# Kernel tuning notes

Measured on AMD Instinct MI355X. Metric: run time of the kernel, lower is better.

## Reference

```python
import jax, jax.numpy as jnp
import numpy as np

B, T, C = 4, 2048, 1024
H, D = 16, 64           # num_heads, head_size
R = D // 2              # rotary_ndims = 32


def _make_rope(T, R):
    # RotaryEmbedding(dim=R): inv_freq over arange(0, R, 2)
    inv_freq = 1.0 / (10000.0 ** (np.arange(0, R, 2, dtype=np.float32) / R))
    t = np.arange(T, dtype=np.float32)
    freqs = np.einsum('i,j->ij', t, inv_freq)        # [T, R/2]
    emb = np.concatenate([freqs, freqs], axis=-1)    # [T, R]
    return jnp.asarray(np.stack([np.cos(emb), np.sin(emb)]), dtype=jnp.float32)  # [2, T, R]


def setup_inputs() -> dict:
    key = jax.random.key(0)
    ks = jax.random.split(key, 10)
    s = 1.0 / np.sqrt(C)
    inp = {
        'x': jax.random.normal(ks[0], (B, T, C), dtype=jnp.float32),
        'RoPE': _make_rope(T, R),
        'key_padding_mask': jax.random.randint(ks[1], (B, T), 0, 2, dtype=jnp.int32),
        'Wq': jax.random.normal(ks[2], (C, C), dtype=jnp.float32) * s,
        'bq': jnp.zeros((C,), dtype=jnp.float32),
        'Wk': jax.random.normal(ks[3], (C, C), dtype=jnp.float32) * s,
        'bk': jnp.zeros((C,), dtype=jnp.float32),
        'Wv': jax.random.normal(ks[4], (C, C), dtype=jnp.float32) * s,
        'bv': jnp.zeros((C,), dtype=jnp.float32),
        'Wo': jax.random.normal(ks[5], (C, C), dtype=jnp.float32) * s,
        'bo': jnp.zeros((C,), dtype=jnp.float32),
    }
    return inp


def _rotate_half(x):
    x1, x2 = x[..., : x.shape[-1] // 2], x[..., x.shape[-1] // 2:]
    return jnp.concatenate([-x2, x1], axis=-1)


def reference(x, RoPE, key_padding_mask, Wq, bq, Wk, bk, Wv, bv, Wo, bo):
    Bx, Tx, Cx = x.shape
    # projections -> [B, H, T, D]
    def proj(W, b):
        return (x @ W.T + b).reshape(Bx, Tx, H, D).transpose(0, 2, 1, 3)
    q, k, v = proj(Wq, bq), proj(Wk, bk), proj(Wv, bv)

    # partial rotary: first R dims rotated, rest passed through
    q_rot, q_pass = q[..., :R], q[..., R:]
    k_rot, k_pass = k[..., :R], k[..., R:]
    cos, sin = RoPE[0][:Tx], RoPE[1][:Tx]            # [T, R]
    q_rot = q_rot * cos + _rotate_half(q_rot) * sin
    k_rot = k_rot * cos + _rotate_half(k_rot) * sin
    q = jnp.concatenate([q_rot, q_pass], axis=-1)
    k = jnp.concatenate([k_rot, k_pass], axis=-1)

    att = jnp.einsum('bhqd,bhkd->bhqk', q, k) * (1.0 / np.sqrt(D))
    mask = key_padding_mask[:, None, None, :]        # [B,1,1,T]
    att = jnp.where(mask == 0, jnp.asarray(-1e30, att.dtype), att)
    att = jax.nn.softmax(att, axis=-1)
    out = jnp.einsum('bhqk,bhkd->bhqd', att, v)      # [B,H,T,D]
    out = out.transpose(0, 2, 1, 3).reshape(Bx, Tx, Cx)
    return out @ Wo.T + bo
```

## Files before the change

kernel.cpp:

```cpp
#include <hip/hip_runtime.h>
#include <stdint.h>


typedef __attribute__((ext_vector_type(8))) short bf16x8;
typedef __attribute__((ext_vector_type(4))) float f32x4;
typedef __attribute__((ext_vector_type(4))) short short4v;
typedef __attribute__((ext_vector_type(2))) uint32_t uint2v;

#define MFMA16(a, b, c) __builtin_amdgcn_mfma_f32_16x16x32_bf16((a), (b), (c), 0, 0, 0)

#if __has_builtin(__builtin_amdgcn_exp2f)
#define FEXP(x) __builtin_amdgcn_exp2f(x)
#define QSCALE 0.18033688011112042f
#else
#define FEXP(x) __expf(x)
#define QSCALE 0.125f
#endif

static __device__ __forceinline__ short f2bf(float f) {
  union { float fv; uint32_t u; } v; v.fv = f;
  uint32_t r = v.u + 0x7FFFu + ((v.u >> 16) & 1u);
  return (short)(r >> 16);
}

static __device__ __forceinline__ uint32_t pack_trunc(float a, float b) {
  union { float f; uint32_t u; } ua, ub;
  ua.f = a; ub.f = b;
#if __has_builtin(__builtin_amdgcn_perm)
  return __builtin_amdgcn_perm(ub.u, ua.u, 0x07060302u);
#else
  return (ub.u & 0xFFFF0000u) | (ua.u >> 16);
#endif
}

typedef __attribute__((address_space(1))) void as1_void;
typedef __attribute__((address_space(3))) void as3_void;
static __device__ __forceinline__ void gld_lds16(const void* g, void* l) {
  __builtin_amdgcn_global_load_lds((as1_void*)g, (as3_void*)l, 16, 0, 0);
}

__global__ __launch_bounds__(256) void cvt_kernel(
    const float* x, const float* wq, const float* wk, const float* wv,
    const float* wo,
    short* xb, short* wqb, short* wkb, short* wvb, short* wob) {
  int64_t g = (int64_t)blockIdx.x * 256 + threadIdx.x;
  const int64_t NX = 8388608 / 4, NW = 1048576 / 4;
  const float* src;
  short* dst;
  int64_t i;
  if (g < NX)               { src = x;  dst = xb;  i = g; }
  else if (g < NX + NW)     { src = wq; dst = wqb; i = g - NX; }
  else if (g < NX + 2 * NW) { src = wk; dst = wkb; i = g - NX - NW; }
  else if (g < NX + 3 * NW) { src = wv; dst = wvb; i = g - NX - 2 * NW; }
  else                      { src = wo; dst = wob; i = g - NX - 3 * NW; }
  float4 v = ((const float4*)src)[i];
  short4v o;
  o[0] = f2bf(v.x); o[1] = f2bf(v.y); o[2] = f2bf(v.z); o[3] = f2bf(v.w);
  *(short4v*)&dst[i * 4] = o;
}

__global__ __launch_bounds__(256, 2) void qkv3_gemm(
    const short* __restrict__ Xb,
    const short* __restrict__ Wq, const short* __restrict__ Wk,
    const short* __restrict__ Wv,
    const float* __restrict__ bq, const float* __restrict__ bk,
    const float* __restrict__ bv,
    const float* __restrict__ rope, const int* __restrict__ mask,
    short* __restrict__ Qh, short* __restrict__ Kh, short* __restrict__ Vt) {
  __shared__ __align__(16) short As[2][128 * 32];
  __shared__ __align__(16) short Bs[2][3][128 * 32];

  const int t = threadIdx.x;
  const int lane = t & 63;
  const int wave = t >> 6;
  const int c = lane & 15;
  const int quad = lane >> 4;
  const int m0 = blockIdx.x * 128;
  const int n0 = blockIdx.y * 128;

  f32x4 zero4 = {0.f, 0.f, 0.f, 0.f};
  f32x4 acc[3][4][4];
#pragma unroll
  for (int m = 0; m < 3; ++m)
#pragma unroll
    for (int i = 0; i < 4; ++i)
#pragma unroll
      for (int j = 0; j < 4; ++j) acc[m][i][j] = zero4;

  const int wm = wave & 1, wn = wave >> 1;

  const int srow = t >> 2;
  const int gc = ((t & 3) - (srow >> 2)) & 3;
  const short* gA = Xb + (size_t)(m0 + srow) * 1024 + gc * 8;
  const short* gW0 = Wq + (size_t)(n0 + srow) * 1024 + gc * 8;
  const short* gW1 = Wk + (size_t)(n0 + srow) * 1024 + gc * 8;
  const short* gW2 = Wv + (size_t)(n0 + srow) * 1024 + gc * 8;

#define QKV_STAGE(buf, k0)                                  \
  do {                                                      \
    gld_lds16(gA + (k0), &As[buf][t * 8]);                  \
    gld_lds16(gA + (k0) + 65536, &As[buf][t * 8 + 2048]);   \
    gld_lds16(gW0 + (k0), &Bs[buf][0][t * 8]);              \
    gld_lds16(gW0 + (k0) + 65536, &Bs[buf][0][t * 8 + 2048]); \
    gld_lds16(gW1 + (k0), &Bs[buf][1][t * 8]);              \
    gld_lds16(gW1 + (k0) + 65536, &Bs[buf][1][t * 8 + 2048]); \
    gld_lds16(gW2 + (k0), &Bs[buf][2][t * 8]);              \
    gld_lds16(gW2 + (k0) + 65536, &Bs[buf][2][t * 8 + 2048]); \
  } while (0)

  QKV_STAGE(0, 0);

  for (int ki = 0; ki < 32; ++ki) {
    __syncthreads();
    if (ki < 31) QKV_STAGE((ki + 1) & 1, (ki + 1) * 32);

    const short* as = &As[ki & 1][0];
    bf16x8 af[4];
#pragma unroll
    for (int i = 0; i < 4; ++i) {
      int mr = wm * 64 + i * 16 + c;
      af[i] = *(const bf16x8*)&as[mr * 32 + (((quad + (mr >> 2)) & 3) * 8)];
    }
#pragma unroll
    for (int m = 0; m < 3; ++m) {
      const short* bs = &Bs[ki & 1][m][0];
      bf16x8 bfr[4];
#pragma unroll
      for (int j = 0; j < 4; ++j) {
        int nr = wn * 64 + j * 16 + c;
        bfr[j] = *(const bf16x8*)&bs[nr * 32 + (((quad + (nr >> 2)) & 3) * 8)];
      }
#pragma unroll
      for (int i = 0; i < 4; ++i)
#pragma unroll
        for (int j = 0; j < 4; ++j)
          acc[m][i][j] = MFMA16(af[i], bfr[j], acc[m][i][j]);
    }
  }
#undef QKV_STAGE

  const int nb = n0 + wn * 64;
  const int hcol = nb >> 6;
  const int bidx = m0 >> 11;
  const int tbase = (m0 & 2047) + wm * 64 + quad * 4;
  const int* mrow = mask + bidx * 2048;

#pragma unroll
  for (int mat = 0; mat < 2; ++mat) {
    short* Og = (mat == 0) ? Qh : Kh;
    const float* bias = (mat == 0) ? bq : bk;
    float bj[4];
#pragma unroll
    for (int j = 0; j < 4; ++j) bj[j] = bias[nb + j * 16 + c];
    size_t hb = (size_t)(bidx * 16 + hcol) * 2048;
#pragma unroll
    for (int i = 0; i < 4; ++i) {
#pragma unroll
      for (int r = 0; r < 4; ++r) {
        int tp = tbase + i * 16 + r;
        float f = (mat == 0) ? QSCALE : (mrow[tp] ? 1.0f : 0.0f);
        float cosv = rope[tp * 32 + c];
        float sinv = rope[65536 + tp * 32 + c];
        float v0 = acc[mat][i][0][r] + bj[0];
        float v1 = acc[mat][i][1][r] + bj[1];
        float v2 = acc[mat][i][2][r] + bj[2];
        float v3 = acc[mat][i][3][r] + bj[3];
        size_t base = (hb + tp) * 64;
        Og[base + c]      = f2bf((v0 * cosv - v1 * sinv) * f);
        Og[base + 16 + c] = f2bf((v1 * cosv + v0 * sinv) * f);
        Og[base + 32 + c] = f2bf(v2 * f);
        Og[base + 48 + c] = f2bf(v3 * f);
      }
    }
  }
  {
    float bj[4];
#pragma unroll
    for (int j = 0; j < 4; ++j) bj[j] = bv[nb + j * 16 + c];
    size_t hb = (size_t)(bidx * 16 + hcol) * 64;
#pragma unroll
    for (int i = 0; i < 4; ++i) {
      int tp = tbase + i * 16;
      int4 mv = *(const int4*)&mrow[tp];
      float fr[4];
      fr[0] = mv.x ? 1.f : 0.f; fr[1] = mv.y ? 1.f : 0.f;
      fr[2] = mv.z ? 1.f : 0.f; fr[3] = mv.w ? 1.f : 0.f;
#pragma unroll
      for (int j = 0; j < 4; ++j) {
        short4v pv;
#pragma unroll
        for (int r = 0; r < 4; ++r)
          pv[r] = f2bf((acc[2][i][j][r] + bj[j]) * fr[r]);
        size_t base = (hb + j * 16 + c) * 2048 + tp;
        *(short4v*)&Vt[base] = pv;
      }
    }
  }
}

__global__ __launch_bounds__(256, 4) void attn_kernel(
    const short* __restrict__ Qh, const short* __restrict__ Kh,
    const short* __restrict__ Vt, const int* __restrict__ mask,
    short* __restrict__ Og) {
  __shared__ __align__(16) short Ks[2][64 * 64];
  __shared__ __align__(16) short Vs[2][64 * 64];
  __shared__ __align__(16) short Pl[4][16 * 64];

  const int t = threadIdx.x;
  const int lane = t & 63;
  const int wave = t >> 6;
  const int c = lane & 15;
  const int quad = lane >> 4;
  const int bh = blockIdx.x;
  const int qt = blockIdx.y;
  const int bidx = bh >> 4;
  const short* Qg = Qh + ((size_t)bh * 2048 + qt * 128) * 64;
  const short* Kg = Kh + (size_t)bh * 2048 * 64;
  const short* Vg = Vt + (size_t)bh * 64 * 2048;

  float nm;
  {
    const int4* mr = (const int4*)(mask + bidx * 2048);
    int cnt = 0;
#pragma unroll
    for (int k = 0; k < 8; ++k) {
      int4 a = mr[k * 64 + lane];
      cnt += (a.x == 0) + (a.y == 0) + (a.z == 0) + (a.w == 0);
    }
    cnt += __shfl_xor(cnt, 1);  cnt += __shfl_xor(cnt, 2);
    cnt += __shfl_xor(cnt, 4);  cnt += __shfl_xor(cnt, 8);
    cnt += __shfl_xor(cnt, 16); cnt += __shfl_xor(cnt, 32);
    nm = (float)cnt;
  }

  bf16x8 qf[2][2];
#pragma unroll
  for (int ks = 0; ks < 2; ++ks)
#pragma unroll
    for (int it = 0; it < 2; ++it)
      qf[ks][it] =
          *(const bf16x8*)&Qg[(wave * 32 + it * 16 + c) * 64 + ks * 32 + quad * 8];

  const bf16x8 ones = {0x3F80, 0x3F80, 0x3F80, 0x3F80,
                       0x3F80, 0x3F80, 0x3F80, 0x3F80};

  f32x4 zero4 = {0.f, 0.f, 0.f, 0.f};
  f32x4 O[4][2];
#pragma unroll
  for (int dt = 0; dt < 4; ++dt)
#pragma unroll
    for (int it = 0; it < 2; ++it) O[dt][it] = zero4;
  f32x4 Ol[2] = {zero4, zero4};

  const int krow0 = t >> 3;
  const int klc = (t & 7) ^ (krow0 & 7);
  const short* gk0 = Kg + (size_t)krow0 * 64 + klc * 8;
  const short* gv0 = Vg + (size_t)krow0 * 2048 + klc * 8;
  short* Pw = &Pl[wave][0];

  gld_lds16(gk0, &Ks[0][t * 8]);
  gld_lds16(gk0 + 32 * 64, &Ks[0][t * 8 + 2048]);
  gld_lds16(gv0, &Vs[0][t * 8]);
  gld_lds16(gv0 + 32 * 2048, &Vs[0][t * 8 + 2048]);

  for (int ci = 0; ci < 32; ++ci) {
    __syncthreads();
    if (ci < 31) {
      int cn = (ci + 1) * 64;
      int nb = (ci + 1) & 1;
      gld_lds16(gk0 + (size_t)cn * 64, &Ks[nb][t * 8]);
      gld_lds16(gk0 + (size_t)(cn + 32) * 64, &Ks[nb][t * 8 + 2048]);
      gld_lds16(gv0 + cn, &Vs[nb][t * 8]);
      gld_lds16(gv0 + cn + 32 * 2048, &Vs[nb][t * 8 + 2048]);
    }
    const short* ksb = &Ks[ci & 1][0];
    const short* vsb = &Vs[ci & 1][0];

    bf16x8 ak[2][4], av[2][4];
#pragma unroll
    for (int ks = 0; ks < 2; ++ks)
#pragma unroll
      for (int jt = 0; jt < 4; ++jt) {
        ak[ks][jt] = *(const bf16x8*)&ksb[(jt * 16 + c) * 64 +
                                          (((4 * ks + quad) ^ (c & 7)) * 8)];
        av[ks][jt] = *(const bf16x8*)&vsb[(jt * 16 + c) * 64 +
                                          (((4 * ks + quad) ^ (c & 7)) * 8)];
      }

#pragma unroll
    for (int it = 0; it < 2; ++it) {
      f32x4 St[4];
#pragma unroll
      for (int jt = 0; jt < 4; ++jt)
        St[jt] = MFMA16(ak[0][jt], qf[0][it], zero4);
#pragma unroll
      for (int jt = 0; jt < 4; ++jt)
        St[jt] = MFMA16(ak[1][jt], qf[1][it], St[jt]);

#pragma unroll
      for (int jt = 0; jt < 4; ++jt) {
        float p0 = FEXP(St[jt][0]);
        float p1 = FEXP(St[jt][1]);
        float p2 = FEXP(St[jt][2]);
        float p3 = FEXP(St[jt][3]);
        uint2v pk;
        pk[0] = pack_trunc(p0, p1);
        pk[1] = pack_trunc(p2, p3);
        *(uint2v*)&Pw[c * 64 +
                      (((jt * 2 + (quad >> 1)) ^ (c & 7)) * 8) +
                      (quad & 1) * 4] = pk;
      }
      asm volatile("s_waitcnt lgkmcnt(0)" ::: "memory");

#pragma unroll
      for (int ks = 0; ks < 2; ++ks) {
        bf16x8 bp =
            *(const bf16x8*)&Pw[c * 64 + (((ks * 4 + quad) ^ (c & 7)) * 8)];
        Ol[it] = MFMA16(ones, bp, Ol[it]);
#pragma unroll
        for (int dt = 0; dt < 4; ++dt)
          O[dt][it] = MFMA16(av[ks][dt], bp, O[dt][it]);
      }
    }
  }

#pragma unroll
  for (int it = 0; it < 2; ++it) {
    float inv = 1.0f / (Ol[it][0] - nm);
    int tq = qt * 128 + wave * 32 + it * 16 + c;
    size_t rb = ((size_t)bidx * 2048 + tq) * 1024 + (size_t)(bh & 15) * 64;
#pragma unroll
    for (int dt = 0; dt < 4; ++dt) {
      short4v ov;
#pragma unroll
      for (int r = 0; r < 4; ++r) ov[r] = f2bf(O[dt][it][r] * inv);
      *(short4v*)&Og[rb + dt * 16 + quad * 4] = ov;
    }
  }
}

__global__ __launch_bounds__(256) void out_gemm(
    const short* __restrict__ Ab, const short* __restrict__ Wob,
    const float* __restrict__ bo, float* __restrict__ out) {
  __shared__ __align__(16) short As[2][64 * 32];
  __shared__ __align__(16) short Bs[2][128 * 32];

  const int t = threadIdx.x;
  const int lane = t & 63;
  const int wave = t >> 6;
  const int c = lane & 15;
  const int quad = lane >> 4;
  const int m0 = blockIdx.x * 64;
  const int n0 = blockIdx.y * 128;

  f32x4 zero4 = {0.f, 0.f, 0.f, 0.f};
  f32x4 acc[4][2];
#pragma unroll
  for (int i = 0; i < 4; ++i) {
    acc[i][0] = zero4;
    acc[i][1] = zero4;
  }

  const int srow = t >> 2;
  const int gc = ((t & 3) - (srow >> 2)) & 3;
  const short* gA = Ab + (size_t)(m0 + srow) * 1024 + gc * 8;
  const short* gB = Wob + (size_t)(n0 + srow) * 1024 + gc * 8;

#define OUT_STAGE(buf, k0)                                   \
  do {                                                       \
    gld_lds16(gA + (k0), &As[buf][t * 8]);                   \
    gld_lds16(gB + (k0), &Bs[buf][t * 8]);                   \
    gld_lds16(gB + (k0) + 65536, &Bs[buf][t * 8 + 2048]);    \
  } while (0)

  OUT_STAGE(0, 0);

  for (int ki = 0; ki < 32; ++ki) {
    __syncthreads();
    if (ki < 31) OUT_STAGE((ki + 1) & 1, (ki + 1) * 32);

    const short* as = &As[ki & 1][0];
    const short* bs = &Bs[ki & 1][0];
    bf16x8 af[4], bfr[2];
#pragma unroll
    for (int i = 0; i < 4; ++i) {
      int mr = i * 16 + c;
      af[i] = *(const bf16x8*)&as[mr * 32 + (((quad + (mr >> 2)) & 3) * 8)];
    }
#pragma unroll
    for (int j = 0; j < 2; ++j) {
      int nr = wave * 32 + j * 16 + c;
      bfr[j] = *(const bf16x8*)&bs[nr * 32 + (((quad + (nr >> 2)) & 3) * 8)];
    }
#pragma unroll
    for (int i = 0; i < 4; ++i) {
      acc[i][0] = MFMA16(af[i], bfr[0], acc[i][0]);
      acc[i][1] = MFMA16(af[i], bfr[1], acc[i][1]);
    }
  }
#undef OUT_STAGE

  const int nb = n0 + wave * 32;
  float bj[2];
  bj[0] = bo[nb + c];
  bj[1] = bo[nb + 16 + c];
#pragma unroll
  for (int i = 0; i < 4; ++i) {
    int m = m0 + i * 16 + quad * 4;
#pragma unroll
    for (int r = 0; r < 4; ++r) {
      float* orow = out + (size_t)(m + r) * 1024 + nb;
      orow[c]      = acc[i][0][r] + bj[0];
      orow[16 + c] = acc[i][1][r] + bj[1];
    }
  }
}

extern "C" void kernel_launch(void* const* d_in, const int* in_sizes, int n_in,
                              void* d_out, int out_size, void* d_ws,
                              size_t ws_size, hipStream_t stream) {
  const float* x    = (const float*)d_in[0];
  const float* rope = (const float*)d_in[1];
  const int*   mask = (const int*)d_in[2];
  const float* Wq   = (const float*)d_in[3];
  const float* bq   = (const float*)d_in[4];
  const float* Wk   = (const float*)d_in[5];
  const float* bk   = (const float*)d_in[6];
  const float* Wv   = (const float*)d_in[7];
  const float* bv   = (const float*)d_in[8];
  const float* Wo   = (const float*)d_in[9];
  const float* bo   = (const float*)d_in[10];
  float* out = (float*)d_out;

  char* ws = (char*)d_ws;
  short* xb  = (short*)(ws);
  short* wqb = (short*)(ws + 16777216);
  short* wkb = (short*)(ws + 18874368);
  short* wvb = (short*)(ws + 20971520);
  short* wob = (short*)(ws + 23068672);
  short* Qh  = (short*)(ws + 25198592);
  short* Kh  = (short*)(ws + 41975808);
  short* Vt  = (short*)(ws + 58753024);
  short* att = xb;

  cvt_kernel<<<12288, 256, 0, stream>>>(x, Wq, Wk, Wv, Wo, xb, wqb, wkb, wvb,
                                        wob);
  qkv3_gemm<<<dim3(64, 8), 256, 0, stream>>>(xb, wqb, wkb, wvb, bq, bk, bv,
                                             rope, mask, Qh, Kh, Vt);
  attn_kernel<<<dim3(64, 16), 256, 0, stream>>>(Qh, Kh, Vt, mask, att);
  out_gemm<<<dim3(128, 8), 256, 0, stream>>>(att, wob, bo, out);
}
```

Measured before the change: 275.9 us.

## Keep softmax probabilities in registers and double query rows per attention block

The attention kernel stops staging exponentiated scores through a per-wave LDS buffer. It packs them directly into MFMA B-operand registers and instead permutes how V is read from LDS, using two half-vector loads, so the lane layout matches. Each block now handles 256 query rows instead of 128, with half as many blocks, so every K/V tile loaded into LDS is reused across twice as many queries. The cost is more accumulator registers, a lower occupancy target of 2 blocks per CU, and fewer blocks overall to fill the GPU.

```diff
diff --git a/kernel.cpp b/kernel.cpp
--- a/kernel.cpp
+++ b/kernel.cpp
@@ -5,7 +5,6 @@
 typedef __attribute__((ext_vector_type(8))) short bf16x8;
 typedef __attribute__((ext_vector_type(4))) float f32x4;
 typedef __attribute__((ext_vector_type(4))) short short4v;
-typedef __attribute__((ext_vector_type(2))) uint32_t uint2v;
 
 #define MFMA16(a, b, c) __builtin_amdgcn_mfma_f32_16x16x32_bf16((a), (b), (c), 0, 0, 0)
 
@@ -198,13 +197,12 @@
   }
 }
 
-__global__ __launch_bounds__(256, 4) void attn_kernel(
+__global__ __launch_bounds__(256, 2) void attn_kernel(
     const short* __restrict__ Qh, const short* __restrict__ Kh,
     const short* __restrict__ Vt, const int* __restrict__ mask,
     short* __restrict__ Og) {
   __shared__ __align__(16) short Ks[2][64 * 64];
   __shared__ __align__(16) short Vs[2][64 * 64];
-  __shared__ __align__(16) short Pl[4][16 * 64];
 
   const int t = threadIdx.x;
   const int lane = t & 63;
@@ -214,7 +212,7 @@
   const int bh = blockIdx.x;
   const int qt = blockIdx.y;
   const int bidx = bh >> 4;
-  const short* Qg = Qh + ((size_t)bh * 2048 + qt * 128) * 64;
+  const short* Qg = Qh + ((size_t)bh * 2048 + qt * 256) * 64;
   const short* Kg = Kh + (size_t)bh * 2048 * 64;
   const short* Vg = Vt + (size_t)bh * 64 * 2048;
 
@@ -233,35 +231,36 @@
     nm = (float)cnt;
   }
 
-  bf16x8 qf[2][2];
+  bf16x8 qf[2][4];
 #pragma unroll
   for (int ks = 0; ks < 2; ++ks)
 #pragma unroll
-    for (int it = 0; it < 2; ++it)
+    for (int it = 0; it < 4; ++it)
       qf[ks][it] =
-          *(const bf16x8*)&Qg[(wave * 32 + it * 16 + c) * 64 + ks * 32 + quad * 8];
+          *(const bf16x8*)&Qg[(wave * 64 + it * 16 + c) * 64 + ks * 32 + quad * 8];
 
   const bf16x8 ones = {0x3F80, 0x3F80, 0x3F80, 0x3F80,
                        0x3F80, 0x3F80, 0x3F80, 0x3F80};
 
   f32x4 zero4 = {0.f, 0.f, 0.f, 0.f};
-  f32x4 O[4][2];
+  f32x4 O[4][4];
 #pragma unroll
   for (int dt = 0; dt < 4; ++dt)
 #pragma unroll
-    for (int it = 0; it < 2; ++it) O[dt][it] = zero4;
-  f32x4 Ol[2] = {zero4, zero4};
+    for (int it = 0; it < 4; ++it) O[dt][it] = zero4;
+  f32x4 Ol[4] = {zero4, zero4, zero4, zero4};
 
   const int krow0 = t >> 3;
   const int klc = (t & 7) ^ (krow0 & 7);
   const short* gk0 = Kg + (size_t)krow0 * 64 + klc * 8;
   const short* gv0 = Vg + (size_t)krow0 * 2048 + klc * 8;
-  short* Pw = &Pl[wave][0];
 
   gld_lds16(gk0, &Ks[0][t * 8]);
   gld_lds16(gk0 + 32 * 64, &Ks[0][t * 8 + 2048]);
   gld_lds16(gv0, &Vs[0][t * 8]);
   gld_lds16(gv0 + 32 * 2048, &Vs[0][t * 8 + 2048]);
+
+  const int s2 = (c & 7) * 2;
 
   for (int ci = 0; ci < 32; ++ci) {
     __syncthreads();
@@ -276,19 +275,30 @@
     const short* ksb = &Ks[ci & 1][0];
     const short* vsb = &Vs[ci & 1][0];
 
-    bf16x8 ak[2][4], av[2][4];
+    bf16x8 ak[2][4];
 #pragma unroll
     for (int ks = 0; ks < 2; ++ks)
 #pragma unroll
-      for (int jt = 0; jt < 4; ++jt) {
+      for (int jt = 0; jt < 4; ++jt)
         ak[ks][jt] = *(const bf16x8*)&ksb[(jt * 16 + c) * 64 +
                                           (((4 * ks + quad) ^ (c & 7)) * 8)];
-        av[ks][jt] = *(const bf16x8*)&vsb[(jt * 16 + c) * 64 +
-                                          (((4 * ks + quad) ^ (c & 7)) * 8)];
-      }
-
-#pragma unroll
-    for (int it = 0; it < 2; ++it) {
+
+    bf16x8 av[2][4];
+#pragma unroll
+    for (int ks = 0; ks < 2; ++ks)
+#pragma unroll
+      for (int dt = 0; dt < 4; ++dt) {
+        int u = (8 * ks + quad) ^ s2;
+        int rowb = (dt * 16 + c) * 64;
+        short4v lo = *(const short4v*)&vsb[rowb + u * 4];
+        short4v hi = *(const short4v*)&vsb[rowb + (u ^ 4) * 4];
+        union { short4v h[2]; bf16x8 v; } uu;
+        uu.h[0] = lo; uu.h[1] = hi;
+        av[ks][dt] = uu.v;
+      }
+
+#pragma unroll
+    for (int it = 0; it < 4; ++it) {
       f32x4 St[4];
 #pragma unroll
       for (int jt = 0; jt < 4; ++jt)
@@ -297,37 +307,31 @@
       for (int jt = 0; jt < 4; ++jt)
         St[jt] = MFMA16(ak[1][jt], qf[1][it], St[jt]);
 
-#pragma unroll
-      for (int jt = 0; jt < 4; ++jt) {
-        float p0 = FEXP(St[jt][0]);
-        float p1 = FEXP(St[jt][1]);
-        float p2 = FEXP(St[jt][2]);
-        float p3 = FEXP(St[jt][3]);
-        uint2v pk;
-        pk[0] = pack_trunc(p0, p1);
-        pk[1] = pack_trunc(p2, p3);
-        *(uint2v*)&Pw[c * 64 +
-                      (((jt * 2 + (quad >> 1)) ^ (c & 7)) * 8) +
-                      (quad & 1) * 4] = pk;
-      }
-      asm volatile("s_waitcnt lgkmcnt(0)" ::: "memory");
-
+      bf16x8 bp[2];
 #pragma unroll
       for (int ks = 0; ks < 2; ++ks) {
-        bf16x8 bp =
-            *(const bf16x8*)&Pw[c * 64 + (((ks * 4 + quad) ^ (c & 7)) * 8)];
-        Ol[it] = MFMA16(ones, bp, Ol[it]);
+        union { uint32_t w[4]; bf16x8 v; } uu;
+        uu.w[0] = pack_trunc(FEXP(St[2 * ks][0]),     FEXP(St[2 * ks][1]));
+        uu.w[1] = pack_trunc(FEXP(St[2 * ks][2]),     FEXP(St[2 * ks][3]));
+        uu.w[2] = pack_trunc(FEXP(St[2 * ks + 1][0]), FEXP(St[2 * ks + 1][1]));
+        uu.w[3] = pack_trunc(FEXP(St[2 * ks + 1][2]), FEXP(St[2 * ks + 1][3]));
+        bp[ks] = uu.v;
+      }
+
+#pragma unroll
+      for (int ks = 0; ks < 2; ++ks) {
+        Ol[it] = MFMA16(ones, bp[ks], Ol[it]);
 #pragma unroll
         for (int dt = 0; dt < 4; ++dt)
-          O[dt][it] = MFMA16(av[ks][dt], bp, O[dt][it]);
-      }
-    }
-  }
-
-#pragma unroll
-  for (int it = 0; it < 2; ++it) {
+          O[dt][it] = MFMA16(av[ks][dt], bp[ks], O[dt][it]);
+      }
+    }
+  }
+
+#pragma unroll
+  for (int it = 0; it < 4; ++it) {
     float inv = 1.0f / (Ol[it][0] - nm);
-    int tq = qt * 128 + wave * 32 + it * 16 + c;
+    int tq = qt * 256 + wave * 64 + it * 16 + c;
     size_t rb = ((size_t)bidx * 2048 + tq) * 1024 + (size_t)(bh & 15) * 64;
 #pragma unroll
     for (int dt = 0; dt < 4; ++dt) {
@@ -447,6 +451,6 @@
                                         wob);
   qkv3_gemm<<<dim3(64, 8), 256, 0, stream>>>(xb, wqb, wkb, wvb, bq, bk, bv,
                                              rope, mask, Qh, Kh, Vt);
-  attn_kernel<<<dim3(64, 16), 256, 0, stream>>>(Qh, Kh, Vt, mask, att);
+  attn_kernel<<<dim3(64, 8), 256, 0, stream>>>(Qh, Kh, Vt, mask, att);
   out_gemm<<<dim3(128, 8), 256, 0, stream>>>(att, wob, bo, out);
 }
```

New measurement: 264.2 us. 1.04x faster.
